# Optimization experiments

Hardware: AMD Instinct MI355X
Metric: run time of the kernel (lower is better)

Reference implementation:

```python
import jax, jax.numpy as jnp
import numpy as np

N, D, H = 4096, 256, 8
DH = D // H
E = 131072
LN_EPS = 1e-5
NEG = -1e9


def setup_inputs() -> dict:
    key = jax.random.key(0)
    ks = jax.random.split(key, 10)
    s = 0.02
    return {
        "embeddings": jax.random.normal(ks[0], (N, D), dtype=jnp.float32),
        "edge_index": jax.random.randint(ks[1], (2, E), 0, N, dtype=jnp.int64),
        "in_proj_w": jax.random.normal(ks[2], (3 * D, D), dtype=jnp.float32) * s,
        "in_proj_b": jnp.zeros((3 * D,), jnp.float32),
        "out_w": jax.random.normal(ks[3], (D, D), dtype=jnp.float32) * s,
        "out_b": jnp.zeros((D,), jnp.float32),
        "lin_w": jax.random.normal(ks[4], (D, D), dtype=jnp.float32) * s,
        "lin_b": jnp.zeros((D,), jnp.float32),
        "ln_g": jnp.ones((D,), jnp.float32),
        "ln_beta": jnp.zeros((D,), jnp.float32),
    }


def reference(embeddings, edge_index, in_proj_w, in_proj_b, out_w, out_b, lin_w, lin_b, ln_g, ln_beta):
    n, d = embeddings.shape
    src, dst = edge_index[0], edge_index[1]
    # symmetric adjacency (per-cell neighbor set = unique nodes touching the cell),
    # self excluded (matches `neighbor_indices != cell_idx`)
    adj = jnp.zeros((n, n), dtype=bool).at[src, dst].set(True).at[dst, src].set(True)
    adj = adj & ~jnp.eye(n, dtype=bool)
    has_nb = adj.any(axis=1)  # [N]

    # MultiheadAttention (eval: dropout off), single query per cell over its neighbors
    qkv = embeddings @ in_proj_w.T + in_proj_b          # [N, 3D]
    q, k, v = jnp.split(qkv, 3, axis=-1)
    qh = q.reshape(n, H, DH)
    kh = k.reshape(n, H, DH)
    vh = v.reshape(n, H, DH)
    scale = 1.0 / np.sqrt(DH).astype(np.float32)
    scores = jnp.einsum('nhd,mhd->nhm', qh, kh) * scale  # [N, H, N]
    scores = jnp.where(adj[:, None, :], scores, NEG)
    attn = jax.nn.softmax(scores, axis=-1)
    ctx = jnp.einsum('nhm,mhd->nhd', attn, vh).reshape(n, d)
    ctx = ctx @ out_w.T + out_b
    # cells with no neighbors keep their own embedding
    x = jnp.where(has_nb[:, None], ctx, embeddings)

    # context_transform: Linear -> LayerNorm -> GELU (dropout off in eval)
    y = x @ lin_w.T + lin_b
    mu = y.mean(axis=-1, keepdims=True)
    var = y.var(axis=-1, keepdims=True)
    y = (y - mu) / jnp.sqrt(var + LN_EPS) * ln_g + ln_beta
    return jax.nn.gelu(y, approximate=False)
```

## Files before the change

### kernel.cpp

```cpp
#include <hip/hip_runtime.h>
#include <math.h>

#define NN 4096
#define DD 256
#define EE 131072
#define MAXD 128
#define SP 132

typedef __attribute__((ext_vector_type(8))) short short8;
typedef __attribute__((ext_vector_type(4))) float float4v;

__device__ __forceinline__ unsigned short f2bf(float f){
    unsigned u = __float_as_uint(f);
    return (unsigned short)((u + 0x7fffu + ((u >> 16) & 1u)) >> 16);
}
__device__ __forceinline__ float blo(unsigned u){ return __uint_as_float(u << 16); }
__device__ __forceinline__ float bhi(unsigned u){ return __uint_as_float(u & 0xffff0000u); }

__device__ __forceinline__ void pack_one(const float* __restrict__ src, unsigned short* __restrict__ dst, int e){
    int lane = e & 63;
    int row = ((e >> 9) << 4) + (lane & 15);
    int k0 = ((e >> 6) & 7) * 32 + ((lane >> 4) << 3);
    const float* p = src + row * DD + k0;
    short8 v;
    #pragma unroll
    for (int j = 0; j < 8; ++j) v[j] = (short)f2bf(p[j]);
    ((short8*)dst)[e] = v;
}

__global__ void k_packw(const float* __restrict__ ipw, const float* __restrict__ ow, const float* __restrict__ lw,
                        unsigned short* __restrict__ bipw, unsigned short* __restrict__ bow,
                        unsigned short* __restrict__ blw, unsigned* __restrict__ adj){
    int e = blockIdx.x * 256 + threadIdx.x;
    for (int i = e; i < 524288; i += 40960) adj[i] = 0u;
    if (e < 24576)       pack_one(ipw, bipw, e);
    else if (e < 32768)  pack_one(ow,  bow,  e - 24576);
    else                 pack_one(lw,  blw,  e - 32768);
}

__global__ void k_edges(const int* __restrict__ ei, unsigned* __restrict__ adj){
    int e = blockIdx.x * 256 + threadIdx.x;
    int s = ei[e];
    int d = ei[EE + e];
    if (s != d){
        atomicOr(&adj[s * 128 + (d >> 5)], 1u << (d & 31));
        atomicOr(&adj[d * 128 + (s >> 5)], 1u << (s & 31));
    }
}

__global__ void __launch_bounds__(256) k_gqkv(const float* __restrict__ emb, const unsigned short* __restrict__ Bp,
                                              const float* __restrict__ bias, float* __restrict__ qf,
                                              unsigned short* __restrict__ kb, unsigned short* __restrict__ vb){
    __shared__ float sA[16 * 260];
    int bx = blockIdx.x, by = blockIdx.y;
    int t = threadIdx.x, w = t >> 6, lane = t & 63;
    #pragma unroll
    for (int i = 0; i < 16; ++i)
        sA[i * 260 + t] = emb[(bx * 16 + i) * 256 + t];
    __syncthreads();

    int arow = lane & 15, ak0 = (lane >> 4) << 3;
    short8 af[8];
    #pragma unroll
    for (int s = 0; s < 8; ++s){
        const float* p = &sA[arow * 260 + s * 32 + ak0];
        #pragma unroll
        for (int j = 0; j < 8; ++j) af[s][j] = (short)f2bf(p[j]);
    }

    const short8* B8 = (const short8*)Bp;
    float4v acc[4];
    #pragma unroll
    for (int c = 0; c < 4; ++c) acc[c] = (float4v){0.f, 0.f, 0.f, 0.f};
    #pragma unroll
    for (int s = 0; s < 8; ++s){
        #pragma unroll
        for (int c = 0; c < 4; ++c){
            int to = by * 16 + w * 4 + c;
            acc[c] = __builtin_amdgcn_mfma_f32_16x16x32_bf16(af[s], B8[(to * 8 + s) * 64 + lane], acc[c], 0, 0, 0);
        }
    }
    int q = lane >> 4, col = lane & 15;
    #pragma unroll
    for (int c = 0; c < 4; ++c){
        int o = (w * 4 + c) * 16 + col;
        float bo = bias[by * 256 + o];
        #pragma unroll
        for (int r = 0; r < 4; ++r){
            int node = bx * 16 + q * 4 + r;
            float val = acc[c][r] + bo;
            if (by == 0)      qf[node * 256 + o] = val;
            else if (by == 1) kb[node * 256 + o] = f2bf(val);
            else              vb[node * 256 + o] = f2bf(val);
        }
    }
}

__device__ __forceinline__ float dot32(const float4* qa, uint4 a, uint4 b, uint4 c, uint4 d){
    float s;
    s  = qa[0].x*blo(a.x) + qa[0].y*bhi(a.x) + qa[0].z*blo(a.y) + qa[0].w*bhi(a.y);
    s += qa[1].x*blo(a.z) + qa[1].y*bhi(a.z) + qa[1].z*blo(a.w) + qa[1].w*bhi(a.w);
    s += qa[2].x*blo(b.x) + qa[2].y*bhi(b.x) + qa[2].z*blo(b.y) + qa[2].w*bhi(b.y);
    s += qa[3].x*blo(b.z) + qa[3].y*bhi(b.z) + qa[3].z*blo(b.w) + qa[3].w*bhi(b.w);
    s += qa[4].x*blo(c.x) + qa[4].y*bhi(c.x) + qa[4].z*blo(c.y) + qa[4].w*bhi(c.y);
    s += qa[5].x*blo(c.z) + qa[5].y*bhi(c.z) + qa[5].z*blo(c.w) + qa[5].w*bhi(c.w);
    s += qa[6].x*blo(d.x) + qa[6].y*bhi(d.x) + qa[6].z*blo(d.y) + qa[6].w*bhi(d.y);
    s += qa[7].x*blo(d.z) + qa[7].y*bhi(d.z) + qa[7].z*blo(d.w) + qa[7].w*bhi(d.w);
    return s;
}

__global__ void __launch_bounds__(128) k_attn(const float* __restrict__ qf, const unsigned short* __restrict__ kb,
                                              const unsigned short* __restrict__ vb, const unsigned* __restrict__ adj,
                                              int* __restrict__ deg, unsigned short* __restrict__ cpk){
    __shared__ int   sNbr[2][MAXD];
    __shared__ float sS[2][8][SP];
    __shared__ float sInv[2][8];
    int wv = threadIdx.x >> 6, lane = threadIdx.x & 63;
    int n = blockIdx.x * 2 + wv;

    uint2 aw = ((const uint2*)(adj + n * 128))[lane];
    int cnt = __popc(aw.x) + __popc(aw.y);
    int pre = cnt;
    #pragma unroll
    for (int off = 1; off < 64; off <<= 1){
        int tmp = __shfl_up(pre, off);
        if (lane >= off) pre += tmp;
    }
    int tot = __shfl(pre, 63);
    int dg = (tot < MAXD) ? tot : MAXD;
    if (lane == 63) deg[n] = dg;
    int base = pre - cnt;
    int mb = lane * 64;
    unsigned b0 = aw.x, b1 = aw.y;
    while (b0){ int b = __ffs(b0) - 1; b0 &= b0 - 1u; if (base < MAXD) sNbr[wv][base] = mb + b; base++; }
    mb += 32;
    while (b1){ int b = __ffs(b1) - 1; b1 &= b1 - 1u; if (base < MAXD) sNbr[wv][base] = mb + b; base++; }
    if (dg == 0) return;
    asm volatile("s_waitcnt lgkmcnt(0)" ::: "memory");

    int js = lane >> 3, h = lane & 7;
    float4 qa[8];
    const float4* q4 = (const float4*)(qf + n * 256 + h * 32);
    #pragma unroll
    for (int i = 0; i < 8; ++i) qa[i] = q4[i];
    for (int jb = 0; jb < dg; jb += 16){
        int j0 = jb + js, j1 = jb + 8 + js;
        bool v0 = j0 < dg, v1 = j1 < dg;
        int m0 = v0 ? sNbr[wv][j0] : sNbr[wv][0];
        int m1 = v1 ? sNbr[wv][j1] : sNbr[wv][0];
        const uint4* kr0 = (const uint4*)(kb + m0 * 256) + h * 4;
        const uint4* kr1 = (const uint4*)(kb + m1 * 256) + h * 4;
        uint4 a0 = kr0[0], a1 = kr0[1], a2 = kr0[2], a3 = kr0[3];
        uint4 c0 = kr1[0], c1 = kr1[1], c2 = kr1[2], c3 = kr1[3];
        float s0 = dot32(qa, a0, a1, a2, a3) * 0.17677669529663687f;
        float s1 = dot32(qa, c0, c1, c2, c3) * 0.17677669529663687f;
        if (v0) sS[wv][h][j0] = s0;
        if (v1) sS[wv][h][j1] = s1;
    }
    asm volatile("s_waitcnt lgkmcnt(0)" ::: "memory");

    int h2 = lane >> 3, i2 = lane & 7;
    float m1 = -1e30f;
    for (int j = i2; j < dg; j += 8) m1 = fmaxf(m1, sS[wv][h2][j]);
    m1 = fmaxf(m1, __shfl_xor(m1, 1));
    m1 = fmaxf(m1, __shfl_xor(m1, 2));
    m1 = fmaxf(m1, __shfl_xor(m1, 4));
    float sum = 0.f;
    for (int j = i2; j < dg; j += 8){ float e = __expf(sS[wv][h2][j] - m1); sS[wv][h2][j] = e; sum += e; }
    sum += __shfl_xor(sum, 1);
    sum += __shfl_xor(sum, 2);
    sum += __shfl_xor(sum, 4);
    if (i2 == 0) sInv[wv][h2] = 1.0f / sum;
    asm volatile("s_waitcnt lgkmcnt(0)" ::: "memory");

    int h3 = lane >> 3;
    const uint2* vb2 = (const uint2*)vb;
    float4 O = {0.f, 0.f, 0.f, 0.f};
    int j = 0;
    for (; j + 4 <= dg; j += 4){
        int m0 = sNbr[wv][j], m1_ = sNbr[wv][j + 1], m2 = sNbr[wv][j + 2], m3 = sNbr[wv][j + 3];
        uint2 u0 = vb2[m0 * 64 + lane];
        uint2 u1 = vb2[m1_ * 64 + lane];
        uint2 u2 = vb2[m2 * 64 + lane];
        uint2 u3 = vb2[m3 * 64 + lane];
        float w0 = sS[wv][h3][j], w1 = sS[wv][h3][j + 1], w2 = sS[wv][h3][j + 2], w3 = sS[wv][h3][j + 3];
        O.x += w0 * blo(u0.x) + w1 * blo(u1.x) + w2 * blo(u2.x) + w3 * blo(u3.x);
        O.y += w0 * bhi(u0.x) + w1 * bhi(u1.x) + w2 * bhi(u2.x) + w3 * bhi(u3.x);
        O.z += w0 * blo(u0.y) + w1 * blo(u1.y) + w2 * blo(u2.y) + w3 * blo(u3.y);
        O.w += w0 * bhi(u0.y) + w1 * bhi(u1.y) + w2 * bhi(u2.y) + w3 * bhi(u3.y);
    }
    for (; j < dg; ++j){
        uint2 u = vb2[sNbr[wv][j] * 64 + lane];
        float wgt = sS[wv][h3][j];
        O.x += wgt * blo(u.x); O.y += wgt * bhi(u.x);
        O.z += wgt * blo(u.y); O.w += wgt * bhi(u.y);
    }
    float inv = sInv[wv][h3];

    int d0 = lane * 4;
    int s  = d0 >> 5;
    int l2 = ((d0 >> 3) & 3) * 16 + (n & 15);
    uint2 pk;
    pk.x = (unsigned)f2bf(O.x * inv) | ((unsigned)f2bf(O.y * inv) << 16);
    pk.y = (unsigned)f2bf(O.z * inv) | ((unsigned)f2bf(O.w * inv) << 16);
    ((uint2*)cpk)[(((n >> 4) * 8 + s) * 64 + l2) * 2 + ((d0 & 7) >> 2)] = pk;
}

__global__ void __launch_bounds__(256) k_tail(const unsigned short* __restrict__ Ap, const unsigned short* __restrict__ Bow,
                                              const float* __restrict__ ob, const float* __restrict__ emb,
                                              const int* __restrict__ deg, const unsigned short* __restrict__ Blw,
                                              const float* __restrict__ lb, const float* __restrict__ g,
                                              const float* __restrict__ beta, float* __restrict__ out){
    __shared__ float xs[16 * 264];
    __shared__ short8 sPk[512];
    __shared__ float stat[16][2];
    int bx = blockIdx.x, t = threadIdx.x;
    int w = t >> 6, lane = t & 63;
    const short8* A8 = (const short8*)Ap;
    const short8* B8 = (const short8*)Bow;

    float4v acc[4];
    #pragma unroll
    for (int c = 0; c < 4; ++c) acc[c] = (float4v){0.f, 0.f, 0.f, 0.f};
    #pragma unroll
    for (int s = 0; s < 8; ++s){
        short8 a = A8[(bx * 8 + s) * 64 + lane];
        #pragma unroll
        for (int c = 0; c < 4; ++c)
            acc[c] = __builtin_amdgcn_mfma_f32_16x16x32_bf16(a, B8[((w * 4 + c) * 8 + s) * 64 + lane], acc[c], 0, 0, 0);
    }
    int q = lane >> 4, col = lane & 15;
    #pragma unroll
    for (int c = 0; c < 4; ++c){
        int o = (w * 4 + c) * 16 + col;
        float bo = ob[o];
        #pragma unroll
        for (int r = 0; r < 4; ++r){
            int row = q * 4 + r, node = bx * 16 + row;
            float x = acc[c][r] + bo;
            if (deg[node] == 0) x = emb[node * 256 + o];
            xs[row * 264 + o] = x;
        }
    }
    __syncthreads();

    #pragma unroll
    for (int pp = 0; pp < 2; ++pp){
        int e = t + pp * 256;
        int l2 = e & 63, s = e >> 6;
        int m = l2 & 15, k0 = s * 32 + ((l2 >> 4) << 3);
        short8 v;
        #pragma unroll
        for (int j = 0; j < 8; ++j) v[j] = (short)f2bf(xs[m * 264 + k0 + j]);
        sPk[e] = v;
    }
    __syncthreads();

    const short8* B2 = (const short8*)Blw;
    float4v acc2[4];
    #pragma unroll
    for (int c = 0; c < 4; ++c) acc2[c] = (float4v){0.f, 0.f, 0.f, 0.f};
    #pragma unroll
    for (int s = 0; s < 8; ++s){
        short8 a = sPk[s * 64 + lane];
        #pragma unroll
        for (int c = 0; c < 4; ++c)
            acc2[c] = __builtin_amdgcn_mfma_f32_16x16x32_bf16(a, B2[((w * 4 + c) * 8 + s) * 64 + lane], acc2[c], 0, 0, 0);
    }
    __syncthreads();
    #pragma unroll
    for (int c = 0; c < 4; ++c){
        int o = (w * 4 + c) * 16 + col;
        float bo = lb[o];
        #pragma unroll
        for (int r = 0; r < 4; ++r)
            xs[(q * 4 + r) * 264 + o] = acc2[c][r] + bo;
    }
    __syncthreads();

    int rr = t >> 4, i = t & 15;
    float s1 = 0.f, s2 = 0.f;
    #pragma unroll
    for (int jj = 0; jj < 16; ++jj){ float v = xs[rr * 264 + i + 16 * jj]; s1 += v; s2 += v * v; }
    #pragma unroll
    for (int off = 8; off > 0; off >>= 1){ s1 += __shfl_xor(s1, off); s2 += __shfl_xor(s2, off); }
    if (i == 0){
        float mu = s1 * (1.0f / 256.0f);
        float var = s2 * (1.0f / 256.0f) - mu * mu;
        stat[rr][0] = mu;
        stat[rr][1] = rsqrtf(fmaxf(var, 0.f) + 1e-5f);
    }
    __syncthreads();
    float mu = stat[rr][0], rs = stat[rr][1];
    int nbase = (bx * 16 + rr) * 256;
    #pragma unroll
    for (int jj = 0; jj < 16; ++jj){
        int cc = i + 16 * jj;
        float z = (xs[rr * 264 + cc] - mu) * rs * g[cc] + beta[cc];
        out[nbase + cc] = 0.5f * z * (1.0f + erff(z * 0.70710678118654752f));
    }
}

extern "C" void kernel_launch(void* const* d_in, const int* in_sizes, int n_in,
                              void* d_out, int out_size, void* d_ws, size_t ws_size,
                              hipStream_t stream){
    const float* emb = (const float*)d_in[0];
    const int*   ei  = (const int*)d_in[1];
    const float* ipw = (const float*)d_in[2];
    const float* ipb = (const float*)d_in[3];
    const float* ow  = (const float*)d_in[4];
    const float* ob  = (const float*)d_in[5];
    const float* lw  = (const float*)d_in[6];
    const float* lb  = (const float*)d_in[7];
    const float* g   = (const float*)d_in[8];
    const float* bet = (const float*)d_in[9];

    char* ws = (char*)d_ws;
    unsigned*       adj  = (unsigned*)(ws);
    int*            deg  = (int*)(ws + 2097152);
    unsigned short* bipw = (unsigned short*)(ws + 2113536);
    unsigned short* bow  = (unsigned short*)(ws + 2506752);
    unsigned short* blw  = (unsigned short*)(ws + 2637824);
    float*          qf   = (float*)(ws + 2768896);
    unsigned short* kb   = (unsigned short*)(ws + 6963200);
    unsigned short* vb   = (unsigned short*)(ws + 9060352);
    unsigned short* cpk  = (unsigned short*)(ws + 11157504);

    k_packw<<<160, 256, 0, stream>>>(ipw, ow, lw, bipw, bow, blw, adj);
    k_edges<<<EE / 256, 256, 0, stream>>>(ei, adj);
    k_gqkv <<<dim3(256, 3), 256, 0, stream>>>(emb, bipw, ipb, qf, kb, vb);
    k_attn <<<NN / 2, 128, 0, stream>>>(qf, kb, vb, adj, deg, cpk);
    k_tail <<<256, 256, 0, stream>>>(cpk, bow, ob, emb, deg, blw, lb, g, bet, (float*)d_out);
}
```

Measured before the change: 136.2 us.

## Fuse edge scatter into QKV GEMM and attention into output tail kernel

The adjacency-building edge scatter moves into the QKV projection kernel, and the per-node attention kernel is merged with the output-projection/LayerNorm/GELU tail so the attention context stays in shared memory instead of going through a global buffer. This drops two kernel launches and the global round-trip for the context and degree arrays. In exchange, each 512-thread block handles 16 nodes serially (2 per wave), which lowers attention parallelism to 256 blocks. The V accumulation is also unrolled by 8 for more loads in flight.

```diff
diff --git a/kernel.cpp b/kernel.cpp
--- a/kernel.cpp
+++ b/kernel.cpp
@@ -38,22 +38,23 @@
     else                 pack_one(lw,  blw,  e - 32768);
 }
 
-__global__ void k_edges(const int* __restrict__ ei, unsigned* __restrict__ adj){
-    int e = blockIdx.x * 256 + threadIdx.x;
-    int s = ei[e];
-    int d = ei[EE + e];
-    if (s != d){
-        atomicOr(&adj[s * 128 + (d >> 5)], 1u << (d & 31));
-        atomicOr(&adj[d * 128 + (s >> 5)], 1u << (s & 31));
-    }
-}
-
 __global__ void __launch_bounds__(256) k_gqkv(const float* __restrict__ emb, const unsigned short* __restrict__ Bp,
                                               const float* __restrict__ bias, float* __restrict__ qf,
-                                              unsigned short* __restrict__ kb, unsigned short* __restrict__ vb){
+                                              unsigned short* __restrict__ kb, unsigned short* __restrict__ vb,
+                                              const int* __restrict__ ei, unsigned* __restrict__ adj){
     __shared__ float sA[16 * 260];
     int bx = blockIdx.x, by = blockIdx.y;
     int t = threadIdx.x, w = t >> 6, lane = t & 63;
+
+    int gid = (by * gridDim.x + bx) * 256 + t;
+    if (gid < EE){
+        int s = ei[gid], d = ei[EE + gid];
+        if (s != d){
+            atomicOr(&adj[s * 128 + (d >> 5)], 1u << (d & 31));
+            atomicOr(&adj[d * 128 + (s >> 5)], 1u << (s & 31));
+        }
+    }
+
     #pragma unroll
     for (int i = 0; i < 16; ++i)
         sA[i * 260 + t] = emb[(bx * 16 + i) * 256 + t];
@@ -109,168 +110,171 @@
     return s;
 }
 
-__global__ void __launch_bounds__(128) k_attn(const float* __restrict__ qf, const unsigned short* __restrict__ kb,
-                                              const unsigned short* __restrict__ vb, const unsigned* __restrict__ adj,
-                                              int* __restrict__ deg, unsigned short* __restrict__ cpk){
-    __shared__ int   sNbr[2][MAXD];
-    __shared__ float sS[2][8][SP];
-    __shared__ float sInv[2][8];
-    int wv = threadIdx.x >> 6, lane = threadIdx.x & 63;
-    int n = blockIdx.x * 2 + wv;
-
-    uint2 aw = ((const uint2*)(adj + n * 128))[lane];
-    int cnt = __popc(aw.x) + __popc(aw.y);
-    int pre = cnt;
-    #pragma unroll
-    for (int off = 1; off < 64; off <<= 1){
-        int tmp = __shfl_up(pre, off);
-        if (lane >= off) pre += tmp;
-    }
-    int tot = __shfl(pre, 63);
-    int dg = (tot < MAXD) ? tot : MAXD;
-    if (lane == 63) deg[n] = dg;
-    int base = pre - cnt;
-    int mb = lane * 64;
-    unsigned b0 = aw.x, b1 = aw.y;
-    while (b0){ int b = __ffs(b0) - 1; b0 &= b0 - 1u; if (base < MAXD) sNbr[wv][base] = mb + b; base++; }
-    mb += 32;
-    while (b1){ int b = __ffs(b1) - 1; b1 &= b1 - 1u; if (base < MAXD) sNbr[wv][base] = mb + b; base++; }
-    if (dg == 0) return;
-    asm volatile("s_waitcnt lgkmcnt(0)" ::: "memory");
-
-    int js = lane >> 3, h = lane & 7;
-    float4 qa[8];
-    const float4* q4 = (const float4*)(qf + n * 256 + h * 32);
-    #pragma unroll
-    for (int i = 0; i < 8; ++i) qa[i] = q4[i];
-    for (int jb = 0; jb < dg; jb += 16){
-        int j0 = jb + js, j1 = jb + 8 + js;
-        bool v0 = j0 < dg, v1 = j1 < dg;
-        int m0 = v0 ? sNbr[wv][j0] : sNbr[wv][0];
-        int m1 = v1 ? sNbr[wv][j1] : sNbr[wv][0];
-        const uint4* kr0 = (const uint4*)(kb + m0 * 256) + h * 4;
-        const uint4* kr1 = (const uint4*)(kb + m1 * 256) + h * 4;
-        uint4 a0 = kr0[0], a1 = kr0[1], a2 = kr0[2], a3 = kr0[3];
-        uint4 c0 = kr1[0], c1 = kr1[1], c2 = kr1[2], c3 = kr1[3];
-        float s0 = dot32(qa, a0, a1, a2, a3) * 0.17677669529663687f;
-        float s1 = dot32(qa, c0, c1, c2, c3) * 0.17677669529663687f;
-        if (v0) sS[wv][h][j0] = s0;
-        if (v1) sS[wv][h][j1] = s1;
-    }
-    asm volatile("s_waitcnt lgkmcnt(0)" ::: "memory");
-
-    int h2 = lane >> 3, i2 = lane & 7;
-    float m1 = -1e30f;
-    for (int j = i2; j < dg; j += 8) m1 = fmaxf(m1, sS[wv][h2][j]);
-    m1 = fmaxf(m1, __shfl_xor(m1, 1));
-    m1 = fmaxf(m1, __shfl_xor(m1, 2));
-    m1 = fmaxf(m1, __shfl_xor(m1, 4));
-    float sum = 0.f;
-    for (int j = i2; j < dg; j += 8){ float e = __expf(sS[wv][h2][j] - m1); sS[wv][h2][j] = e; sum += e; }
-    sum += __shfl_xor(sum, 1);
-    sum += __shfl_xor(sum, 2);
-    sum += __shfl_xor(sum, 4);
-    if (i2 == 0) sInv[wv][h2] = 1.0f / sum;
-    asm volatile("s_waitcnt lgkmcnt(0)" ::: "memory");
-
-    int h3 = lane >> 3;
-    const uint2* vb2 = (const uint2*)vb;
-    float4 O = {0.f, 0.f, 0.f, 0.f};
-    int j = 0;
-    for (; j + 4 <= dg; j += 4){
-        int m0 = sNbr[wv][j], m1_ = sNbr[wv][j + 1], m2 = sNbr[wv][j + 2], m3 = sNbr[wv][j + 3];
-        uint2 u0 = vb2[m0 * 64 + lane];
-        uint2 u1 = vb2[m1_ * 64 + lane];
-        uint2 u2 = vb2[m2 * 64 + lane];
-        uint2 u3 = vb2[m3 * 64 + lane];
-        float w0 = sS[wv][h3][j], w1 = sS[wv][h3][j + 1], w2 = sS[wv][h3][j + 2], w3 = sS[wv][h3][j + 3];
-        O.x += w0 * blo(u0.x) + w1 * blo(u1.x) + w2 * blo(u2.x) + w3 * blo(u3.x);
-        O.y += w0 * bhi(u0.x) + w1 * bhi(u1.x) + w2 * bhi(u2.x) + w3 * bhi(u3.x);
-        O.z += w0 * blo(u0.y) + w1 * blo(u1.y) + w2 * blo(u2.y) + w3 * blo(u3.y);
-        O.w += w0 * bhi(u0.y) + w1 * bhi(u1.y) + w2 * bhi(u2.y) + w3 * bhi(u3.y);
-    }
-    for (; j < dg; ++j){
-        uint2 u = vb2[sNbr[wv][j] * 64 + lane];
-        float wgt = sS[wv][h3][j];
-        O.x += wgt * blo(u.x); O.y += wgt * bhi(u.x);
-        O.z += wgt * blo(u.y); O.w += wgt * bhi(u.y);
-    }
-    float inv = sInv[wv][h3];
-
-    int d0 = lane * 4;
-    int s  = d0 >> 5;
-    int l2 = ((d0 >> 3) & 3) * 16 + (n & 15);
-    uint2 pk;
-    pk.x = (unsigned)f2bf(O.x * inv) | ((unsigned)f2bf(O.y * inv) << 16);
-    pk.y = (unsigned)f2bf(O.z * inv) | ((unsigned)f2bf(O.w * inv) << 16);
-    ((uint2*)cpk)[(((n >> 4) * 8 + s) * 64 + l2) * 2 + ((d0 & 7) >> 2)] = pk;
-}
-
-__global__ void __launch_bounds__(256) k_tail(const unsigned short* __restrict__ Ap, const unsigned short* __restrict__ Bow,
-                                              const float* __restrict__ ob, const float* __restrict__ emb,
-                                              const int* __restrict__ deg, const unsigned short* __restrict__ Blw,
-                                              const float* __restrict__ lb, const float* __restrict__ g,
-                                              const float* __restrict__ beta, float* __restrict__ out){
-    __shared__ float xs[16 * 264];
+__global__ void __launch_bounds__(512) k_attn_tail(
+        const float* __restrict__ qf, const unsigned short* __restrict__ kb,
+        const unsigned short* __restrict__ vb, const unsigned* __restrict__ adj,
+        const float* __restrict__ emb,
+        const unsigned short* __restrict__ Bow, const float* __restrict__ ob,
+        const unsigned short* __restrict__ Blw, const float* __restrict__ lb,
+        const float* __restrict__ g, const float* __restrict__ beta,
+        float* __restrict__ out){
+    __shared__ float  sS[8][8][SP];
+    __shared__ int    sNbr[8][MAXD];
     __shared__ short8 sPk[512];
-    __shared__ float stat[16][2];
+    __shared__ float  sInv[8][8];
+    __shared__ int    sDeg[16];
+    __shared__ float  stat[16][2];
     int bx = blockIdx.x, t = threadIdx.x;
-    int w = t >> 6, lane = t & 63;
-    const short8* A8 = (const short8*)Ap;
+    int wv = t >> 6, lane = t & 63;
+    int n0 = bx * 16;
+    float* xs = (float*)sS;
+
+    for (int u = 0; u < 2; ++u){
+        int m = wv * 2 + u;
+        int n = n0 + m;
+
+        uint2 aw = ((const uint2*)(adj + n * 128))[lane];
+        int cnt = __popc(aw.x) + __popc(aw.y);
+        int pre = cnt;
+        #pragma unroll
+        for (int off = 1; off < 64; off <<= 1){
+            int tmp = __shfl_up(pre, off);
+            if (lane >= off) pre += tmp;
+        }
+        int tot = __shfl(pre, 63);
+        int dg = (tot < MAXD) ? tot : MAXD;
+        if (lane == 63) sDeg[m] = dg;
+        int base = pre - cnt;
+        int mb = lane * 64;
+        unsigned b0 = aw.x, b1 = aw.y;
+        while (b0){ int b = __ffs(b0) - 1; b0 &= b0 - 1u; if (base < MAXD) sNbr[wv][base] = mb + b; base++; }
+        mb += 32;
+        while (b1){ int b = __ffs(b1) - 1; b1 &= b1 - 1u; if (base < MAXD) sNbr[wv][base] = mb + b; base++; }
+        if (dg == 0) continue;
+        asm volatile("s_waitcnt lgkmcnt(0)" ::: "memory");
+
+        int js = lane >> 3, h = lane & 7;
+        float4 qa[8];
+        const float4* q4 = (const float4*)(qf + n * 256 + h * 32);
+        #pragma unroll
+        for (int i = 0; i < 8; ++i) qa[i] = q4[i];
+        for (int jb = 0; jb < dg; jb += 16){
+            int j0 = jb + js, j1 = jb + 8 + js;
+            bool v0 = j0 < dg, v1 = j1 < dg;
+            int m0 = v0 ? sNbr[wv][j0] : sNbr[wv][0];
+            int m1 = v1 ? sNbr[wv][j1] : sNbr[wv][0];
+            const uint4* kr0 = (const uint4*)(kb + m0 * 256) + h * 4;
+            const uint4* kr1 = (const uint4*)(kb + m1 * 256) + h * 4;
+            uint4 a0 = kr0[0], a1 = kr0[1], a2 = kr0[2], a3 = kr0[3];
+            uint4 c0 = kr1[0], c1 = kr1[1], c2 = kr1[2], c3 = kr1[3];
+            float s0 = dot32(qa, a0, a1, a2, a3) * 0.17677669529663687f;
+            float s1 = dot32(qa, c0, c1, c2, c3) * 0.17677669529663687f;
+            if (v0) sS[wv][h][j0] = s0;
+            if (v1) sS[wv][h][j1] = s1;
+        }
+        asm volatile("s_waitcnt lgkmcnt(0)" ::: "memory");
+
+        int h2 = lane >> 3, i2 = lane & 7;
+        float m1 = -1e30f;
+        for (int j = i2; j < dg; j += 8) m1 = fmaxf(m1, sS[wv][h2][j]);
+        m1 = fmaxf(m1, __shfl_xor(m1, 1));
+        m1 = fmaxf(m1, __shfl_xor(m1, 2));
+        m1 = fmaxf(m1, __shfl_xor(m1, 4));
+        float sum = 0.f;
+        for (int j = i2; j < dg; j += 8){ float e = __expf(sS[wv][h2][j] - m1); sS[wv][h2][j] = e; sum += e; }
+        sum += __shfl_xor(sum, 1);
+        sum += __shfl_xor(sum, 2);
+        sum += __shfl_xor(sum, 4);
+        if (i2 == 0) sInv[wv][h2] = 1.0f / sum;
+        asm volatile("s_waitcnt lgkmcnt(0)" ::: "memory");
+
+        int h3 = lane >> 3;
+        const uint2* vb2 = (const uint2*)vb;
+        float4 O = {0.f, 0.f, 0.f, 0.f};
+        int j = 0;
+        for (; j + 8 <= dg; j += 8){
+            uint2 uu[8]; float ww[8];
+            #pragma unroll
+            for (int k = 0; k < 8; ++k){
+                uu[k] = vb2[sNbr[wv][j + k] * 64 + lane];
+                ww[k] = sS[wv][h3][j + k];
+            }
+            #pragma unroll
+            for (int k = 0; k < 8; ++k){
+                O.x += ww[k] * blo(uu[k].x); O.y += ww[k] * bhi(uu[k].x);
+                O.z += ww[k] * blo(uu[k].y); O.w += ww[k] * bhi(uu[k].y);
+            }
+        }
+        for (; j < dg; ++j){
+            uint2 u = vb2[sNbr[wv][j] * 64 + lane];
+            float wgt = sS[wv][h3][j];
+            O.x += wgt * blo(u.x); O.y += wgt * bhi(u.x);
+            O.z += wgt * blo(u.y); O.w += wgt * bhi(u.y);
+        }
+        float inv = sInv[wv][h3];
+
+        int d0 = lane * 4;
+        int s  = d0 >> 5;
+        int l2 = ((d0 >> 3) & 3) * 16 + m;
+        uint2 pk;
+        pk.x = (unsigned)f2bf(O.x * inv) | ((unsigned)f2bf(O.y * inv) << 16);
+        pk.y = (unsigned)f2bf(O.z * inv) | ((unsigned)f2bf(O.w * inv) << 16);
+        ((uint2*)sPk)[(s * 64 + l2) * 2 + ((d0 & 7) >> 2)] = pk;
+    }
+    __syncthreads();
+
     const short8* B8 = (const short8*)Bow;
-
-    float4v acc[4];
-    #pragma unroll
-    for (int c = 0; c < 4; ++c) acc[c] = (float4v){0.f, 0.f, 0.f, 0.f};
+    float4v acc[2];
+    #pragma unroll
+    for (int c = 0; c < 2; ++c) acc[c] = (float4v){0.f, 0.f, 0.f, 0.f};
     #pragma unroll
     for (int s = 0; s < 8; ++s){
-        short8 a = A8[(bx * 8 + s) * 64 + lane];
-        #pragma unroll
-        for (int c = 0; c < 4; ++c)
-            acc[c] = __builtin_amdgcn_mfma_f32_16x16x32_bf16(a, B8[((w * 4 + c) * 8 + s) * 64 + lane], acc[c], 0, 0, 0);
+        short8 a = sPk[s * 64 + lane];
+        #pragma unroll
+        for (int c = 0; c < 2; ++c)
+            acc[c] = __builtin_amdgcn_mfma_f32_16x16x32_bf16(a, B8[((wv * 2 + c) * 8 + s) * 64 + lane], acc[c], 0, 0, 0);
     }
     int q = lane >> 4, col = lane & 15;
     #pragma unroll
-    for (int c = 0; c < 4; ++c){
-        int o = (w * 4 + c) * 16 + col;
+    for (int c = 0; c < 2; ++c){
+        int o = (wv * 2 + c) * 16 + col;
         float bo = ob[o];
         #pragma unroll
         for (int r = 0; r < 4; ++r){
-            int row = q * 4 + r, node = bx * 16 + row;
+            int row = q * 4 + r;
             float x = acc[c][r] + bo;
-            if (deg[node] == 0) x = emb[node * 256 + o];
+            if (sDeg[row] == 0) x = emb[(n0 + row) * 256 + o];
             xs[row * 264 + o] = x;
         }
     }
     __syncthreads();
 
-    #pragma unroll
-    for (int pp = 0; pp < 2; ++pp){
-        int e = t + pp * 256;
-        int l2 = e & 63, s = e >> 6;
+    {
+        int l2 = t & 63, s = t >> 6;
         int m = l2 & 15, k0 = s * 32 + ((l2 >> 4) << 3);
         short8 v;
         #pragma unroll
         for (int j = 0; j < 8; ++j) v[j] = (short)f2bf(xs[m * 264 + k0 + j]);
-        sPk[e] = v;
+        __syncthreads();
+        sPk[t] = v;
     }
     __syncthreads();
 
     const short8* B2 = (const short8*)Blw;
-    float4v acc2[4];
-    #pragma unroll
-    for (int c = 0; c < 4; ++c) acc2[c] = (float4v){0.f, 0.f, 0.f, 0.f};
+    float4v acc2[2];
+    #pragma unroll
+    for (int c = 0; c < 2; ++c) acc2[c] = (float4v){0.f, 0.f, 0.f, 0.f};
     #pragma unroll
     for (int s = 0; s < 8; ++s){
         short8 a = sPk[s * 64 + lane];
         #pragma unroll
-        for (int c = 0; c < 4; ++c)
-            acc2[c] = __builtin_amdgcn_mfma_f32_16x16x32_bf16(a, B2[((w * 4 + c) * 8 + s) * 64 + lane], acc2[c], 0, 0, 0);
-    }
-    __syncthreads();
-    #pragma unroll
-    for (int c = 0; c < 4; ++c){
-        int o = (w * 4 + c) * 16 + col;
+        for (int c = 0; c < 2; ++c)
+            acc2[c] = __builtin_amdgcn_mfma_f32_16x16x32_bf16(a, B2[((wv * 2 + c) * 8 + s) * 64 + lane], acc2[c], 0, 0, 0);
+    }
+    __syncthreads();
+    #pragma unroll
+    for (int c = 0; c < 2; ++c){
+        int o = (wv * 2 + c) * 16 + col;
         float bo = lb[o];
         #pragma unroll
         for (int r = 0; r < 4; ++r)
@@ -278,12 +282,12 @@
     }
     __syncthreads();
 
-    int rr = t >> 4, i = t & 15;
+    int rr = t >> 5, i = t & 31;
     float s1 = 0.f, s2 = 0.f;
     #pragma unroll
-    for (int jj = 0; jj < 16; ++jj){ float v = xs[rr * 264 + i + 16 * jj]; s1 += v; s2 += v * v; }
-    #pragma unroll
-    for (int off = 8; off > 0; off >>= 1){ s1 += __shfl_xor(s1, off); s2 += __shfl_xor(s2, off); }
+    for (int jj = 0; jj < 8; ++jj){ float v = xs[rr * 264 + i + 32 * jj]; s1 += v; s2 += v * v; }
+    #pragma unroll
+    for (int off = 16; off > 0; off >>= 1){ s1 += __shfl_xor(s1, off); s2 += __shfl_xor(s2, off); }
     if (i == 0){
         float mu = s1 * (1.0f / 256.0f);
         float var = s2 * (1.0f / 256.0f) - mu * mu;
@@ -292,10 +296,10 @@
     }
     __syncthreads();
     float mu = stat[rr][0], rs = stat[rr][1];
-    int nbase = (bx * 16 + rr) * 256;
-    #pragma unroll
-    for (int jj = 0; jj < 16; ++jj){
-        int cc = i + 16 * jj;
+    int nbase = (n0 + rr) * 256;
+    #pragma unroll
+    for (int jj = 0; jj < 8; ++jj){
+        int cc = i + 32 * jj;
         float z = (xs[rr * 264 + cc] - mu) * rs * g[cc] + beta[cc];
         out[nbase + cc] = 0.5f * z * (1.0f + erff(z * 0.70710678118654752f));
     }
@@ -317,18 +321,14 @@
 
     char* ws = (char*)d_ws;
     unsigned*       adj  = (unsigned*)(ws);
-    int*            deg  = (int*)(ws + 2097152);
     unsigned short* bipw = (unsigned short*)(ws + 2113536);
     unsigned short* bow  = (unsigned short*)(ws + 2506752);
     unsigned short* blw  = (unsigned short*)(ws + 2637824);
     float*          qf   = (float*)(ws + 2768896);
     unsigned short* kb   = (unsigned short*)(ws + 6963200);
     unsigned short* vb   = (unsigned short*)(ws + 9060352);
-    unsigned short* cpk  = (unsigned short*)(ws + 11157504);
-
-    k_packw<<<160, 256, 0, stream>>>(ipw, ow, lw, bipw, bow, blw, adj);
-    k_edges<<<EE / 256, 256, 0, stream>>>(ei, adj);
-    k_gqkv <<<dim3(256, 3), 256, 0, stream>>>(emb, bipw, ipb, qf, kb, vb);
-    k_attn <<<NN / 2, 128, 0, stream>>>(qf, kb, vb, adj, deg, cpk);
-    k_tail <<<256, 256, 0, stream>>>(cpk, bow, ob, emb, deg, blw, lb, g, bet, (float*)d_out);
-}
+
+    k_packw    <<<160, 256, 0, stream>>>(ipw, ow, lw, bipw, bow, blw, adj);
+    k_gqkv     <<<dim3(256, 3), 256, 0, stream>>>(emb, bipw, ipb, qf, kb, vb, ei, adj);
+    k_attn_tail<<<256, 512, 0, stream>>>(qf, kb, vb, adj, emb, bow, ob, blw, lb, g, bet, (float*)d_out);
+}
```

Result: faster. 129.7 us (-4.8%).
